# Optimization experiments

Hardware: AMD Instinct MI355X
Metric: run time of the kernel (lower is better)

Reference implementation:

```python
import jax, jax.numpy as jnp
import numpy as np

N, E, H, L, G, C = 50000, 800000, 64, 4, 500, 10
BN_EPS = 1e-5


def setup_inputs() -> dict:
    key = jax.random.key(0)
    ks = jax.random.split(key, 24)
    x = jax.random.normal(ks[0], (N, H), dtype=jnp.float32)
    edge_index = jax.random.randint(ks[1], (2, E), 0, N, dtype=jnp.int64)
    batch = jnp.sort(jax.random.randint(ks[2], (N,), 0, G, dtype=jnp.int64))
    s = 1.0 / np.sqrt(H)
    # stacked per-layer GIN MLP params: Linear->BN->ReLU->Linear->BN->ReLU
    conv_W1 = jax.random.uniform(ks[3], (L, H, H), minval=-s, maxval=s, dtype=jnp.float32)
    conv_b1 = jax.random.uniform(ks[4], (L, H), minval=-s, maxval=s, dtype=jnp.float32)
    bn1_g = jax.random.uniform(ks[5], (L, H), minval=0.5, maxval=1.5, dtype=jnp.float32)
    bn1_b = jax.random.normal(ks[6], (L, H), dtype=jnp.float32) * 0.1
    bn1_m = jax.random.normal(ks[7], (L, H), dtype=jnp.float32) * 0.1
    bn1_v = jax.random.uniform(ks[8], (L, H), minval=0.5, maxval=1.5, dtype=jnp.float32)
    conv_W2 = jax.random.uniform(ks[9], (L, H, H), minval=-s, maxval=s, dtype=jnp.float32)
    conv_b2 = jax.random.uniform(ks[10], (L, H), minval=-s, maxval=s, dtype=jnp.float32)
    bn2_g = jax.random.uniform(ks[11], (L, H), minval=0.5, maxval=1.5, dtype=jnp.float32)
    bn2_b = jax.random.normal(ks[12], (L, H), dtype=jnp.float32) * 0.1
    bn2_m = jax.random.normal(ks[13], (L, H), dtype=jnp.float32) * 0.1
    bn2_v = jax.random.uniform(ks[14], (L, H), minval=0.5, maxval=1.5, dtype=jnp.float32)
    s1 = 1.0 / np.sqrt(L * H)
    lin1_W = jax.random.uniform(ks[15], (L * H, H), minval=-s1, maxval=s1, dtype=jnp.float32)
    lin1_b = jax.random.uniform(ks[16], (H,), minval=-s1, maxval=s1, dtype=jnp.float32)
    lin2_W = jax.random.uniform(ks[17], (H, C), minval=-s, maxval=s, dtype=jnp.float32)
    lin2_b = jax.random.uniform(ks[18], (C,), minval=-s, maxval=s, dtype=jnp.float32)
    return dict(x=x, edge_index=edge_index, batch=batch,
                conv_W1=conv_W1, conv_b1=conv_b1, bn1_g=bn1_g, bn1_b=bn1_b, bn1_m=bn1_m, bn1_v=bn1_v,
                conv_W2=conv_W2, conv_b2=conv_b2, bn2_g=bn2_g, bn2_b=bn2_b, bn2_m=bn2_m, bn2_v=bn2_v,
                lin1_W=lin1_W, lin1_b=lin1_b, lin2_W=lin2_W, lin2_b=lin2_b)


def _bn(h, g, b, m, v):
    # eval-mode BatchNorm1d with running stats
    return g * (h - m) * jax.lax.rsqrt(v + BN_EPS) + b


def reference(x, edge_index, batch,
              conv_W1, conv_b1, bn1_g, bn1_b, bn1_m, bn1_v,
              conv_W2, conv_b2, bn2_g, bn2_b, bn2_m, bn2_v,
              lin1_W, lin1_b, lin2_W, lin2_b):
    src, dst = edge_index[0], edge_index[1]

    def layer(h, p):
        W1, b1, g1, be1, m1, v1, W2, b2, g2, be2, m2, v2 = p
        # GIN aggregation (eps=0): h_i + sum_{j->i} h_j, scatter-add over edges
        agg = jax.ops.segment_sum(h[src], dst, num_segments=N)
        z = h + agg
        z = jax.nn.relu(_bn(z @ W1 + b1, g1, be1, m1, v1))
        z = jax.nn.relu(_bn(z @ W2 + b2, g2, be2, m2, v2))
        return z, z

    params = (conv_W1, conv_b1, bn1_g, bn1_b, bn1_m, bn1_v,
              conv_W2, conv_b2, bn2_g, bn2_b, bn2_m, bn2_v)
    _, xs = jax.lax.scan(layer, x, params)          # [L, N, H]
    xcat = jnp.transpose(xs, (1, 0, 2)).reshape(N, L * H)  # JK 'cat'
    pooled = jax.ops.segment_sum(xcat, batch, num_segments=G)  # sum readout [G, L*H]
    h = jax.nn.relu(pooled @ lin1_W + lin1_b)
    # dropout is identity in eval mode
    return h @ lin2_W + lin2_b  # [G, C]
```

## Files before the change

### kernel.cpp

```cpp
#include <hip/hip_runtime.h>

#define NN 50000
#define NE 800000
#define HH 64
#define LL 4
#define GG 500
#define CC 10
#define BN_EPS 1e-5f
#define SCB 200
#define NPART 6250
#define ECHUNK 2048
#define NCHUNK 391
#define CASTB 3125

typedef short bf16x8 __attribute__((ext_vector_type(8)));
typedef float f32x4  __attribute__((ext_vector_type(4)));

__device__ inline float bf2f(unsigned int u16) {
    union { unsigned int i; float f; } v; v.i = u16 << 16; return v.f;
}
__device__ inline unsigned short f2bf(float f) {
    union { float f; unsigned int i; } v; v.f = f;
    unsigned int u = v.i + 0x7fffu + ((v.i >> 16) & 1u);
    return (unsigned short)(u >> 16);
}
__device__ inline void addrow8(float* acc, uint4 u) {
    #pragma unroll
    for (int q = 0; q < 4; ++q) {
        unsigned int w = (&u.x)[q];
        union { unsigned int i; float f; } lo, hi;
        lo.i = w << 16; hi.i = w & 0xffff0000u;
        acc[2 * q]     += lo.f;
        acc[2 * q + 1] += hi.f;
    }
}

__global__ __launch_bounds__(256) void k_prep(const float* __restrict__ x, unsigned short* __restrict__ xb,
                                              const float* __restrict__ cW1, const float* __restrict__ cW2,
                                              unsigned short* __restrict__ fragW)
{
    if (blockIdx.x < CASTB) {
        int i = blockIdx.x * 256 + threadIdx.x;
        if (i < NN * 16) {
            float4 v = ((const float4*)x)[i];
            uint2 p;
            p.x = (unsigned int)f2bf(v.x) | ((unsigned int)f2bf(v.y) << 16);
            p.y = (unsigned int)f2bf(v.z) | ((unsigned int)f2bf(v.w) << 16);
            ((uint2*)xb)[i] = p;
        }
        return;
    }
    int idx = (blockIdx.x - CASTB) * 256 + threadIdx.x;
    if (idx >= LL * 2 * 4 * 2 * 64 * 8) return;
    int j    = idx & 7;
    int lane = (idx >> 3) & 63;
    int kh   = (idx >> 9) & 1;
    int ct   = (idx >> 10) & 3;
    int g    = (idx >> 12) & 1;
    int L    = idx >> 13;
    int k = kh * 32 + (lane >> 4) * 8 + j;
    int n = ct * 16 + (lane & 15);
    const float* W = (g == 0 ? cW1 : cW2) + (size_t)L * HH * HH;
    float w = W[k * HH + n];
    unsigned short hi = f2bf(w);
    unsigned short lo = f2bf(w - bf2f(hi));
    size_t fhi = ((size_t)L * 32 + ((g * 2 + 0) * 4 + ct) * 2 + kh) * 512 + lane * 8 + j;
    size_t flo = ((size_t)L * 32 + ((g * 2 + 1) * 4 + ct) * 2 + kh) * 512 + lane * 8 + j;
    fragW[fhi] = hi;
    fragW[flo] = lo;
}

__global__ __launch_bounds__(256) void k_hist8(const int* __restrict__ dst, int* __restrict__ deg) {
    int part  = blockIdx.x & 7;
    int chunk = blockIdx.x >> 3;
    int lo = part * NPART, hi = lo + NPART;
    int base = chunk * ECHUNK + threadIdx.x;
    #pragma unroll
    for (int i = 0; i < 8; ++i) {
        int e = base + i * 256;
        if (e < NE) {
            int d = dst[e];
            if (d >= lo && d < hi) atomicAdd(&deg[d], 1);
        }
    }
}

__global__ __launch_bounds__(256) void k_scan1(const int* __restrict__ deg, int* __restrict__ incl,
                                               int* __restrict__ bsum) {
    int t = threadIdx.x;
    int idx = blockIdx.x * 256 + t;
    __shared__ int s[256];
    int v = (idx < NN) ? deg[idx] : 0;
    s[t] = v;
    __syncthreads();
    for (int off = 1; off < 256; off <<= 1) {
        int u = (t >= off) ? s[t - off] : 0;
        __syncthreads();
        if (t >= off) s[t] += u;
        __syncthreads();
    }
    if (idx < NN) incl[idx] = s[t];
    if (t == 255) bsum[blockIdx.x] = s[255];
}

__global__ __launch_bounds__(256) void k_scan3f(const int* __restrict__ deg, const int* __restrict__ incl,
                                                const int* __restrict__ bsum, int* __restrict__ row_ptr) {
    int t = threadIdx.x;
    __shared__ int s[256];
    int v = (t < SCB) ? bsum[t] : 0;
    s[t] = v;
    __syncthreads();
    for (int off = 1; off < 256; off <<= 1) {
        int u = (t >= off) ? s[t - off] : 0;
        __syncthreads();
        if (t >= off) s[t] += u;
        __syncthreads();
    }
    int boff_b = (blockIdx.x == 0) ? 0 : s[blockIdx.x - 1];
    if (blockIdx.x == 0 && t == 0) row_ptr[NN] = s[SCB - 1];
    int idx = blockIdx.x * 256 + t;
    if (idx < NN) row_ptr[idx] = incl[idx] - deg[idx] + boff_b;
}

__global__ __launch_bounds__(256) void k_scatter8(const int* __restrict__ src, const int* __restrict__ dst,
                                                  const int* __restrict__ row_ptr, int* __restrict__ cursor,
                                                  int* __restrict__ col) {
    int part  = blockIdx.x & 7;
    int chunk = blockIdx.x >> 3;
    int lo = part * NPART, hi = lo + NPART;
    int base = chunk * ECHUNK + threadIdx.x;
    #pragma unroll
    for (int i = 0; i < 8; ++i) {
        int e = base + i * 256;
        if (e < NE) {
            int d = dst[e];
            if (d >= lo && d < hi) {
                int pos = atomicAdd(&cursor[d], 1);
                col[row_ptr[d] + pos] = src[e];
            }
        }
    }
}

__global__ __launch_bounds__(256) void k_agg(
    const unsigned short* __restrict__ hb, unsigned short* __restrict__ aggb,
    const int* __restrict__ row_ptr, const int* __restrict__ col)
{
    int tid  = threadIdx.x;
    int lane = tid & 63;
    int wave = tid >> 6;
    int gl   = lane & 7;
    int grp  = lane >> 3;
    int n = blockIdx.x * 32 + wave * 8 + grp;
    if (n >= NN) return;

    const uint4* hv = (const uint4*)hb;
    float acc[8]  = {0.f, 0.f, 0.f, 0.f, 0.f, 0.f, 0.f, 0.f};
    float acc2[8] = {0.f, 0.f, 0.f, 0.f, 0.f, 0.f, 0.f, 0.f};
    addrow8(acc, hv[(size_t)n * 8 + gl]);

    int j = row_ptr[n], fin = row_ptr[n + 1];
    for (; j + 8 <= fin; j += 8) {
        int s0 = col[j],     s1 = col[j + 1], s2 = col[j + 2], s3 = col[j + 3];
        int s4 = col[j + 4], s5 = col[j + 5], s6 = col[j + 6], s7 = col[j + 7];
        uint4 u0 = hv[(size_t)s0 * 8 + gl];
        uint4 u1 = hv[(size_t)s1 * 8 + gl];
        uint4 u2 = hv[(size_t)s2 * 8 + gl];
        uint4 u3 = hv[(size_t)s3 * 8 + gl];
        uint4 u4 = hv[(size_t)s4 * 8 + gl];
        uint4 u5 = hv[(size_t)s5 * 8 + gl];
        uint4 u6 = hv[(size_t)s6 * 8 + gl];
        uint4 u7 = hv[(size_t)s7 * 8 + gl];
        addrow8(acc, u0);  addrow8(acc2, u1);
        addrow8(acc, u2);  addrow8(acc2, u3);
        addrow8(acc, u4);  addrow8(acc2, u5);
        addrow8(acc, u6);  addrow8(acc2, u7);
    }
    for (; j + 4 <= fin; j += 4) {
        int s0 = col[j], s1 = col[j + 1], s2 = col[j + 2], s3 = col[j + 3];
        uint4 u0 = hv[(size_t)s0 * 8 + gl];
        uint4 u1 = hv[(size_t)s1 * 8 + gl];
        uint4 u2 = hv[(size_t)s2 * 8 + gl];
        uint4 u3 = hv[(size_t)s3 * 8 + gl];
        addrow8(acc, u0);  addrow8(acc2, u1);
        addrow8(acc, u2);  addrow8(acc2, u3);
    }
    for (; j < fin; ++j)
        addrow8(acc, hv[(size_t)col[j] * 8 + gl]);

    #pragma unroll
    for (int q = 0; q < 8; ++q) acc[q] += acc2[q];

    uint4 o;
    o.x = (unsigned int)f2bf(acc[0]) | ((unsigned int)f2bf(acc[1]) << 16);
    o.y = (unsigned int)f2bf(acc[2]) | ((unsigned int)f2bf(acc[3]) << 16);
    o.z = (unsigned int)f2bf(acc[4]) | ((unsigned int)f2bf(acc[5]) << 16);
    o.w = (unsigned int)f2bf(acc[6]) | ((unsigned int)f2bf(acc[7]) << 16);
    ((uint4*)(aggb + (size_t)n * HH))[gl] = o;
}

#define MT 128
#define SAB 80
#define SOF 68

__global__ __launch_bounds__(256) void k_mlp2(
    const unsigned short* __restrict__ agg, unsigned short* __restrict__ h_out,
    const int* __restrict__ batch, float* __restrict__ pooled, int layer,
    const unsigned short* __restrict__ fragW,
    const float* __restrict__ lb1, const float* __restrict__ g1,
    const float* __restrict__ bb1, const float* __restrict__ m1, const float* __restrict__ v1,
    const float* __restrict__ lb2, const float* __restrict__ g2,
    const float* __restrict__ bb2, const float* __restrict__ m2, const float* __restrict__ v2)
{
    __shared__ unsigned short sHi[128 * SAB];
    __shared__ unsigned short sLo[128 * SAB];
    __shared__ float sOut[128 * SOF];
    __shared__ float red[256];

    int tid  = threadIdx.x;
    int lane = tid & 63;
    int wave = tid >> 6;
    int l15 = lane & 15, l4 = lane >> 4;
    int base = blockIdx.x * MT;
    int wrow = wave * 32;

    float sc1v[4], sh1v[4], sc2v[4], sh2v[4];
    #pragma unroll
    for (int ct = 0; ct < 4; ++ct) {
        int c = ct * 16 + l15;
        float s1 = g1[c] * rsqrtf(v1[c] + BN_EPS);
        sc1v[ct] = s1; sh1v[ct] = (lb1[c] - m1[c]) * s1 + bb1[c];
        float s2 = g2[c] * rsqrtf(v2[c] + BN_EPS);
        sc2v[ct] = s2; sh2v[ct] = (lb2[c] - m2[c]) * s2 + bb2[c];
    }

    for (int i = tid; i < 128 * 8; i += 256) {
        int r = i >> 3, q = i & 7;
        int gr = base + r;
        uint4 u = (gr < NN) ? ((const uint4*)(agg + (size_t)gr * HH))[q] : make_uint4(0, 0, 0, 0);
        *(uint4*)&sHi[r * SAB + q * 8] = u;
    }
    __syncthreads();

    const bf16x8* fwv = (const bf16x8*)fragW + ((size_t)layer * 32) * 64;

    bf16x8 a0[2][2];
    #pragma unroll
    for (int rt = 0; rt < 2; ++rt)
        #pragma unroll
        for (int kh = 0; kh < 2; ++kh)
            a0[rt][kh] = *(const bf16x8*)&sHi[(wrow + rt * 16 + l15) * SAB + kh * 32 + l4 * 8];

    f32x4 acc[2][4];
    #pragma unroll
    for (int rt = 0; rt < 2; ++rt)
        #pragma unroll
        for (int ct = 0; ct < 4; ++ct) {
            f32x4 c = {0.f, 0.f, 0.f, 0.f};
            #pragma unroll
            for (int kh = 0; kh < 2; ++kh) {
                c = __builtin_amdgcn_mfma_f32_16x16x32_bf16(a0[rt][kh], fwv[((0 * 4 + ct) * 2 + kh) * 64 + lane], c, 0, 0, 0);
                c = __builtin_amdgcn_mfma_f32_16x16x32_bf16(a0[rt][kh], fwv[((1 * 4 + ct) * 2 + kh) * 64 + lane], c, 0, 0, 0);
            }
            acc[rt][ct] = c;
        }
    __syncthreads();

    #pragma unroll
    for (int rt = 0; rt < 2; ++rt)
        #pragma unroll
        for (int ct = 0; ct < 4; ++ct)
            #pragma unroll
            for (int rg = 0; rg < 4; ++rg) {
                int r = wrow + rt * 16 + l4 * 4 + rg;
                float z = fmaxf(fmaf(acc[rt][ct][rg], sc1v[ct], sh1v[ct]), 0.f);
                unsigned short hi = f2bf(z);
                sHi[r * SAB + ct * 16 + l15] = hi;
                sLo[r * SAB + ct * 16 + l15] = f2bf(z - bf2f(hi));
            }
    __syncthreads();

    bf16x8 ah[2][2], al[2][2];
    #pragma unroll
    for (int rt = 0; rt < 2; ++rt)
        #pragma unroll
        for (int kh = 0; kh < 2; ++kh) {
            int off = (wrow + rt * 16 + l15) * SAB + kh * 32 + l4 * 8;
            ah[rt][kh] = *(const bf16x8*)&sHi[off];
            al[rt][kh] = *(const bf16x8*)&sLo[off];
        }
    #pragma unroll
    for (int rt = 0; rt < 2; ++rt)
        #pragma unroll
        for (int ct = 0; ct < 4; ++ct) {
            f32x4 c = {0.f, 0.f, 0.f, 0.f};
            #pragma unroll
            for (int kh = 0; kh < 2; ++kh) {
                bf16x8 bh = fwv[((2 * 4 + ct) * 2 + kh) * 64 + lane];
                bf16x8 bl = fwv[((3 * 4 + ct) * 2 + kh) * 64 + lane];
                c = __builtin_amdgcn_mfma_f32_16x16x32_bf16(ah[rt][kh], bh, c, 0, 0, 0);
                c = __builtin_amdgcn_mfma_f32_16x16x32_bf16(al[rt][kh], bh, c, 0, 0, 0);
                c = __builtin_amdgcn_mfma_f32_16x16x32_bf16(ah[rt][kh], bl, c, 0, 0, 0);
            }
            #pragma unroll
            for (int rg = 0; rg < 4; ++rg) {
                int r = wrow + rt * 16 + l4 * 4 + rg;
                float z = fmaxf(fmaf(c[rg], sc2v[ct], sh2v[ct]), 0.f);
                sOut[r * SOF + ct * 16 + l15] = z;
            }
        }
    __syncthreads();

    for (int i = tid; i < 128 * 8; i += 256) {
        int r = i >> 3, q = i & 7;
        int gr = base + r;
        if (gr < NN) {
            const float* sp = &sOut[r * SOF + q * 8];
            uint4 o;
            o.x = (unsigned int)f2bf(sp[0]) | ((unsigned int)f2bf(sp[1]) << 16);
            o.y = (unsigned int)f2bf(sp[2]) | ((unsigned int)f2bf(sp[3]) << 16);
            o.z = (unsigned int)f2bf(sp[4]) | ((unsigned int)f2bf(sp[5]) << 16);
            o.w = (unsigned int)f2bf(sp[6]) | ((unsigned int)f2bf(sp[7]) << 16);
            ((uint4*)(h_out + (size_t)gr * HH))[q] = o;
        }
    }

    int thi = base + MT; if (thi > NN) thi = NN;
    int gfirst = batch[base];
    int glast  = batch[thi - 1];
    int c = tid & 63;
    int q = tid >> 6;
    for (int g = gfirst; g <= glast; ++g) {
        int lo = base, hb = thi;
        while (lo < hb) { int mid = (lo + hb) >> 1; if (batch[mid] < g) lo = mid + 1; else hb = mid; }
        int lo_g = lo;
        hb = thi;
        while (lo < hb) { int mid = (lo + hb) >> 1; if (batch[mid] < g + 1) lo = mid + 1; else hb = mid; }
        int hi_g = lo;
        float a = 0.f;
        for (int r = lo_g + q; r < hi_g; r += 4) a += sOut[(r - base) * SOF + c];
        red[tid] = a;
        __syncthreads();
        if (tid < 64)
            atomicAdd(&pooled[(size_t)g * (LL * HH) + layer * HH + c],
                      red[c] + red[64 + c] + red[128 + c] + red[192 + c]);
        __syncthreads();
    }
}

__global__ __launch_bounds__(64) void k_mlp(const float* __restrict__ pooled,
                                            const float* __restrict__ w1, const float* __restrict__ b1,
                                            const float* __restrict__ w2, const float* __restrict__ b2,
                                            float* __restrict__ out)
{
    int g = blockIdx.x, c = threadIdx.x;
    __shared__ float hh[64];
    float acc = b1[c];
    const float* p = pooled + g * (LL * HH);
    #pragma unroll 8
    for (int k = 0; k < LL * HH; ++k) acc = fmaf(p[k], w1[k * HH + c], acc);
    hh[c] = fmaxf(acc, 0.f);
    __syncthreads();
    if (c < CC) {
        float o = b2[c];
        #pragma unroll
        for (int k = 0; k < HH; ++k) o = fmaf(hh[k], w2[k * CC + c], o);
        out[g * CC + c] = o;
    }
}

extern "C" void kernel_launch(void* const* d_in, const int* in_sizes, int n_in,
                              void* d_out, int out_size, void* d_ws, size_t ws_size,
                              hipStream_t stream) {
    const float* x    = (const float*)d_in[0];
    const int*   ei   = (const int*)d_in[1];
    const int*   bat  = (const int*)d_in[2];
    const float* cW1  = (const float*)d_in[3];
    const float* cb1  = (const float*)d_in[4];
    const float* g1   = (const float*)d_in[5];
    const float* bb1  = (const float*)d_in[6];
    const float* m1   = (const float*)d_in[7];
    const float* v1   = (const float*)d_in[8];
    const float* cW2  = (const float*)d_in[9];
    const float* cb2  = (const float*)d_in[10];
    const float* g2   = (const float*)d_in[11];
    const float* bb2  = (const float*)d_in[12];
    const float* m2   = (const float*)d_in[13];
    const float* v2   = (const float*)d_in[14];
    const float* l1W  = (const float*)d_in[15];
    const float* l1b  = (const float*)d_in[16];
    const float* l2W  = (const float*)d_in[17];
    const float* l2b  = (const float*)d_in[18];

    const int* srcp = ei;
    const int* dstp = ei + NE;

    char* ws = (char*)d_ws;
    size_t off = 0;
    auto alloc = [&](size_t bytes) -> char* {
        char* p = ws + off;
        off += (bytes + 255) & ~size_t(255);
        return p;
    };
    unsigned short* xb    = (unsigned short*)alloc((size_t)NN * HH * 2);
    unsigned short* hb0   = (unsigned short*)alloc((size_t)NN * HH * 2);
    unsigned short* hb1   = (unsigned short*)alloc((size_t)NN * HH * 2);
    unsigned short* aggb  = (unsigned short*)alloc((size_t)NN * HH * 2);
    unsigned short* fragW = (unsigned short*)alloc((size_t)LL * 32 * 512 * 2);
    int*   deg     = (int*)alloc((size_t)NN * sizeof(int));
    int*   cursor  = (int*)alloc((size_t)NN * sizeof(int));
    float* pooled  = (float*)alloc((size_t)GG * LL * HH * sizeof(float));
    size_t zspan   = (size_t)((char*)(pooled + (size_t)GG * LL * HH) - (char*)deg);
    int*   row_ptr = (int*)alloc((size_t)(NN + 1) * sizeof(int));
    int*   incl    = (int*)alloc((size_t)NN * sizeof(int));
    int*   colx    = (int*)alloc((size_t)NE * sizeof(int));
    int*   bsum    = (int*)alloc(256 * sizeof(int));

    hipMemsetAsync(deg, 0, zspan, stream);

    k_hist8<<<8 * NCHUNK, 256, 0, stream>>>(dstp, deg);
    k_prep<<<CASTB + 128, 256, 0, stream>>>(x, xb, cW1, cW2, fragW);
    k_scan1<<<SCB, 256, 0, stream>>>(deg, incl, bsum);
    k_scan3f<<<SCB, 256, 0, stream>>>(deg, incl, bsum, row_ptr);
    k_scatter8<<<8 * NCHUNK, 256, 0, stream>>>(srcp, dstp, row_ptr, cursor, colx);

    const unsigned short* hin = xb;
    unsigned short* bufs[2] = { hb0, hb1 };
    const int AGG_BLK = (NN + 31) / 32;
    const int MLP_BLK = (NN + MT - 1) / MT;
    for (int l = 0; l < LL; ++l) {
        unsigned short* hout = bufs[l & 1];
        k_agg<<<AGG_BLK, 256, 0, stream>>>(hin, aggb, row_ptr, colx);
        k_mlp2<<<MLP_BLK, 256, 0, stream>>>(aggb, hout, bat, pooled, l, fragW,
            cb1 + l * HH, g1 + l * HH, bb1 + l * HH, m1 + l * HH, v1 + l * HH,
            cb2 + l * HH, g2 + l * HH, bb2 + l * HH, m2 + l * HH, v2 + l * HH);
        hin = hout;
    }

    k_mlp<<<GG, 64, 0, stream>>>(pooled, l1W, l1b, l2W, l2b, (float*)d_out);
}
```

Before: 314.5 us.

## Split node features into two column halves and aggregate each half in separate passes

Result: slower. 337.6 us (+7.3%).

```diff
diff --git a/kernel.cpp b/kernel.cpp
--- a/kernel.cpp
+++ b/kernel.cpp
@@ -12,9 +12,11 @@
 #define ECHUNK 2048
 #define NCHUNK 391
 #define CASTB 3125
+#define AGGB2 782
 
 typedef short bf16x8 __attribute__((ext_vector_type(8)));
 typedef float f32x4  __attribute__((ext_vector_type(4)));
+typedef unsigned int u32x4 __attribute__((ext_vector_type(4)));
 
 __device__ inline float bf2f(unsigned int u16) {
     union { unsigned int i; float f; } v; v.i = u16 << 16; return v.f;
@@ -46,7 +48,9 @@
             uint2 p;
             p.x = (unsigned int)f2bf(v.x) | ((unsigned int)f2bf(v.y) << 16);
             p.y = (unsigned int)f2bf(v.z) | ((unsigned int)f2bf(v.w) << 16);
-            ((uint2*)xb)[i] = p;
+            int n = i >> 4, cq = i & 15;
+            int half = cq >> 3, c8 = cq & 7;
+            ((uint2*)xb)[((size_t)half * NN + n) * 8 + c8] = p;
         }
         return;
     }
@@ -142,61 +146,48 @@
     }
 }
 
-__global__ __launch_bounds__(256) void k_agg(
+__global__ __launch_bounds__(256) void k_agg2(
     const unsigned short* __restrict__ hb, unsigned short* __restrict__ aggb,
     const int* __restrict__ row_ptr, const int* __restrict__ col)
 {
     int tid  = threadIdx.x;
     int lane = tid & 63;
     int wave = tid >> 6;
-    int gl   = lane & 7;
-    int grp  = lane >> 3;
-    int n = blockIdx.x * 32 + wave * 8 + grp;
+    int gl   = lane & 3;
+    int grp  = lane >> 2;
+    int bid  = blockIdx.x;
+    int pass = 0;
+    if (bid >= AGGB2) { pass = 1; bid -= AGGB2; }
+    int n = bid * 64 + wave * 16 + grp;
     if (n >= NN) return;
 
-    const uint4* hv = (const uint4*)hb;
+    const uint4* hv = (const uint4*)(hb + (size_t)pass * NN * 32);
     float acc[8]  = {0.f, 0.f, 0.f, 0.f, 0.f, 0.f, 0.f, 0.f};
     float acc2[8] = {0.f, 0.f, 0.f, 0.f, 0.f, 0.f, 0.f, 0.f};
-    addrow8(acc, hv[(size_t)n * 8 + gl]);
+    addrow8(acc, hv[(size_t)n * 4 + gl]);
 
     int j = row_ptr[n], fin = row_ptr[n + 1];
-    for (; j + 8 <= fin; j += 8) {
-        int s0 = col[j],     s1 = col[j + 1], s2 = col[j + 2], s3 = col[j + 3];
-        int s4 = col[j + 4], s5 = col[j + 5], s6 = col[j + 6], s7 = col[j + 7];
-        uint4 u0 = hv[(size_t)s0 * 8 + gl];
-        uint4 u1 = hv[(size_t)s1 * 8 + gl];
-        uint4 u2 = hv[(size_t)s2 * 8 + gl];
-        uint4 u3 = hv[(size_t)s3 * 8 + gl];
-        uint4 u4 = hv[(size_t)s4 * 8 + gl];
-        uint4 u5 = hv[(size_t)s5 * 8 + gl];
-        uint4 u6 = hv[(size_t)s6 * 8 + gl];
-        uint4 u7 = hv[(size_t)s7 * 8 + gl];
+    for (; j + 4 <= fin; j += 4) {
+        int s0 = col[j], s1 = col[j + 1], s2 = col[j + 2], s3 = col[j + 3];
+        uint4 u0 = hv[(size_t)s0 * 4 + gl];
+        uint4 u1 = hv[(size_t)s1 * 4 + gl];
+        uint4 u2 = hv[(size_t)s2 * 4 + gl];
+        uint4 u3 = hv[(size_t)s3 * 4 + gl];
         addrow8(acc, u0);  addrow8(acc2, u1);
         addrow8(acc, u2);  addrow8(acc2, u3);
-        addrow8(acc, u4);  addrow8(acc2, u5);
-        addrow8(acc, u6);  addrow8(acc2, u7);
-    }
-    for (; j + 4 <= fin; j += 4) {
-        int s0 = col[j], s1 = col[j + 1], s2 = col[j + 2], s3 = col[j + 3];
-        uint4 u0 = hv[(size_t)s0 * 8 + gl];
-        uint4 u1 = hv[(size_t)s1 * 8 + gl];
-        uint4 u2 = hv[(size_t)s2 * 8 + gl];
-        uint4 u3 = hv[(size_t)s3 * 8 + gl];
-        addrow8(acc, u0);  addrow8(acc2, u1);
-        addrow8(acc, u2);  addrow8(acc2, u3);
     }
     for (; j < fin; ++j)
-        addrow8(acc, hv[(size_t)col[j] * 8 + gl]);
+        addrow8(acc, hv[(size_t)col[j] * 4 + gl]);
 
     #pragma unroll
     for (int q = 0; q < 8; ++q) acc[q] += acc2[q];
 
-    uint4 o;
+    u32x4 o;
     o.x = (unsigned int)f2bf(acc[0]) | ((unsigned int)f2bf(acc[1]) << 16);
     o.y = (unsigned int)f2bf(acc[2]) | ((unsigned int)f2bf(acc[3]) << 16);
     o.z = (unsigned int)f2bf(acc[4]) | ((unsigned int)f2bf(acc[5]) << 16);
     o.w = (unsigned int)f2bf(acc[6]) | ((unsigned int)f2bf(acc[7]) << 16);
-    ((uint4*)(aggb + (size_t)n * HH))[gl] = o;
+    __builtin_nontemporal_store(o, (u32x4*)(aggb + (size_t)n * HH) + (pass * 4 + gl));
 }
 
 #define MT 128
@@ -321,7 +312,8 @@
             o.y = (unsigned int)f2bf(sp[2]) | ((unsigned int)f2bf(sp[3]) << 16);
             o.z = (unsigned int)f2bf(sp[4]) | ((unsigned int)f2bf(sp[5]) << 16);
             o.w = (unsigned int)f2bf(sp[6]) | ((unsigned int)f2bf(sp[7]) << 16);
-            ((uint4*)(h_out + (size_t)gr * HH))[q] = o;
+            int half = q >> 2, qq = q & 3;
+            ((uint4*)h_out)[((size_t)half * NN + gr) * 4 + qq] = o;
         }
     }
 
@@ -416,7 +408,7 @@
     int*   colx    = (int*)alloc((size_t)NE * sizeof(int));
     int*   bsum    = (int*)alloc(256 * sizeof(int));
 
-    hipMemsetAsync(deg, 0, zspan, stream);
+    (void)hipMemsetAsync(deg, 0, zspan, stream);
 
     k_hist8<<<8 * NCHUNK, 256, 0, stream>>>(dstp, deg);
     k_prep<<<CASTB + 128, 256, 0, stream>>>(x, xb, cW1, cW2, fragW);
@@ -426,11 +418,10 @@
 
     const unsigned short* hin = xb;
     unsigned short* bufs[2] = { hb0, hb1 };
-    const int AGG_BLK = (NN + 31) / 32;
     const int MLP_BLK = (NN + MT - 1) / MT;
     for (int l = 0; l < LL; ++l) {
         unsigned short* hout = bufs[l & 1];
-        k_agg<<<AGG_BLK, 256, 0, stream>>>(hin, aggb, row_ptr, colx);
+        k_agg2<<<2 * AGGB2, 256, 0, stream>>>(hin, aggb, row_ptr, colx);
         k_mlp2<<<MLP_BLK, 256, 0, stream>>>(aggb, hout, bat, pooled, l, fragW,
             cb1 + l * HH, g1 + l * HH, bb1 + l * HH, m1 + l * HH, v1 + l * HH,
             cb2 + l * HH, g2 + l * HH, bb2 + l * HH, m2 + l * HH, v2 + l * HH);
```
